# Performance work log

Measured on AMD Instinct MI355X. Metric: run time of the kernel, lower is better.

The kernel has to match this reference:

```python
import jax, jax.numpy as jnp
import numpy as np

ITERS = 8
LAMBDA0 = 0.01
PAD = 1.0
LR = 1.0
EPS = 1e-12


def _sobel_grads(fmap):
    # kornia spatial_gradient: normalized 3x3 sobel (/8), replicate padding. fmap: C,H,W
    kx = jnp.array([[-1., 0., 1.], [-2., 0., 2.], [-1., 0., 1.]], fmap.dtype) / 8.0
    k = jnp.stack([kx, kx.T])[:, None]                       # 2,1,3,3 (OIHW)
    f = jnp.pad(fmap, ((0, 0), (1, 1), (1, 1)), mode='edge')[:, None]  # C,1,H+2,W+2
    g = jax.lax.conv_general_dilated(f, k, (1, 1), 'VALID')  # C,2,H,W
    return g[:, 0], g[:, 1]


def _bilinear(tensor, pts):
    # grid_sample bilinear, align_corners=True, at pixel coords. tensor: C,H,W; pts: N,2 (x,y) -> N,C
    c, h, w = tensor.shape
    x, y = pts[:, 0], pts[:, 1]
    x0 = jnp.clip(jnp.floor(x), 0, w - 1)
    y0 = jnp.clip(jnp.floor(y), 0, h - 1)
    x1 = jnp.clip(x0 + 1, 0, w - 1)
    y1 = jnp.clip(y0 + 1, 0, h - 1)
    wx, wy = x - x0, y - y0
    x0i, x1i = x0.astype(jnp.int32), x1.astype(jnp.int32)
    y0i, y1i = y0.astype(jnp.int32), y1.astype(jnp.int32)
    v00 = tensor[:, y0i, x0i]
    v01 = tensor[:, y0i, x1i]
    v10 = tensor[:, y1i, x0i]
    v11 = tensor[:, y1i, x1i]
    out = (v00 * (1 - wx) * (1 - wy) + v01 * wx * (1 - wy)
           + v10 * (1 - wx) * wy + v11 * wx * wy)
    return out.T


def _skew(v):
    x, y, z = v[..., 0], v[..., 1], v[..., 2]
    o = jnp.zeros_like(x)
    return jnp.stack([o, -z, y, z, o, -x, -y, x, o], -1).reshape(v.shape[:-1] + (3, 3))


def _so3exp(w):
    theta = jnp.linalg.norm(w)
    small = theta < 1e-7
    th = jnp.where(small, 1.0, theta)
    A = jnp.where(small, 1.0, jnp.sin(th) / th)
    B = jnp.where(small, 0.5, (1.0 - jnp.cos(th)) / th ** 2)
    W = _skew(w)
    return jnp.eye(3, dtype=w.dtype) + A * W + B * (W @ W)


def _normalize(x):
    return x / jnp.maximum(jnp.linalg.norm(x, axis=-1, keepdims=True), EPS)


def _pnp(p3D, feature_ref, feature_query, K, R_init, t_init):
    C, H, W = feature_query.shape
    gx, gy = _sobel_grads(feature_query)
    fref = _normalize(feature_ref)
    fx, fy, cx, cy = K[0, 0], K[1, 1], K[0, 2], K[1, 2]
    f_scale = jnp.stack([fx, fy])
    c_off = jnp.stack([cx, cy])

    def project(R, t):
        p3q = p3D @ R.T + t
        pn = p3q[:, :2] / p3q[:, 2:3]
        return p3q, pn, pn * f_scale + c_off

    def in_image(p2):
        return ((p2[:, 0] >= PAD) & (p2[:, 0] < W - PAD)
                & (p2[:, 1] >= PAD) & (p2[:, 1] < H - PAD))

    def masked_cost(p2, vf):
        f = _normalize(_bilinear(feature_query, p2))
        cost = ((f - fref) ** 2).sum(-1)
        return (cost * vf).sum() / vf.sum()

    R, t = R_init, t_init
    lam = jnp.asarray(LAMBDA0, p3D.dtype)
    jacobi = None
    cost_best = None
    p2D_init = None

    for i in range(ITERS):
        p3q, pn, p2 = project(R, t)
        if i == 0:
            p2D_init = jax.lax.stop_gradient(p2)
        vf = in_image(p2).astype(p3D.dtype)  # mask-weight == gather of valid pts

        f_raw = _bilinear(feature_query, p2)  # N,C
        norm = jnp.maximum(jnp.linalg.norm(f_raw, axis=-1, keepdims=True), EPS)
        f = f_raw / norm
        error = f - fref
        if i == 0:
            cost_best = (((error ** 2).sum(-1)) * vf).sum() / vf.sum()

        # Jacobian chain: J = J_f_p2 @ J_p2_pn @ J_pn_p3 @ J_p3_T   -> N,C,6
        x_, y_, d = p3q[:, 0], p3q[:, 1], p3q[:, 2]
        z = jnp.zeros_like(d)
        Jpn = jnp.stack([1 / d, z, -x_ / d ** 2,
                         z, 1 / d, -y_ / d ** 2], -1).reshape(-1, 2, 3)
        Jpn = Jpn * f_scale[None, :, None]  # fold in J_p2_pn = diag(fx,fy)
        Jp3T = jnp.concatenate(
            [jnp.broadcast_to(jnp.eye(3, dtype=p3D.dtype), p3q.shape[:-1] + (3, 3)),
             -_skew(p3q)], -1)  # N,3,6
        J26 = Jpn @ Jp3T       # N,2,6

        Jf = jnp.stack([_bilinear(gx, p2), _bilinear(gy, p2)], -1)  # N,C,2
        # normalize-feat Jacobian (I - f f^T)/||f_raw||, fused (no NxCxC)
        proj = jnp.einsum('nc,nck->nk', f, Jf)
        Jf = (Jf - f[:, :, None] * proj[:, None, :]) / norm[:, :, None]

        J = Jf @ J26  # N,C,6
        if i == 0:
            jacobi = 1.0 / (1.0 + jnp.linalg.norm(J * vf[:, None, None], axis=(0, 1)))
        J = J * jacobi

        Grad = jnp.einsum('ncj,nc,n->j', J, error, vf)
        Hess = jnp.einsum('nci,ncj,n->ij', J, J, vf)

        damp = jnp.diag(jnp.diagonal(Hess) + 1e-9) * lam  # LM damping
        delta = -LR * jnp.linalg.solve(Hess + damp, Grad)
        delta = delta * jacobi
        dt, dw = delta[:3], delta[3:6]
        dr = _so3exp(dw)
        R_new, t_new = dr @ R, dr @ t + dt

        _, _, p2_new = project(R_new, t_new)
        vf_new = in_image(p2_new).astype(p3D.dtype)
        cost_new = masked_cost(p2_new, vf_new)

        accept = cost_new <= cost_best
        lam = jnp.clip(lam * jnp.where(accept, 0.1, 10.0), 1e-8, 1e4)
        R = jnp.where(accept, R_new, R)
        t = jnp.where(accept, t_new, t)
        cost_best = jnp.where(accept, cost_new, cost_best)

    p3D_sg = jax.lax.stop_gradient(p3D)
    pf = p3D_sg @ R.T + t
    p2f = (pf[:, :2] / pf[:, 2:3]) * f_scale + c_off
    f_i = _normalize(_bilinear(feature_query, p2D_init))
    f_f = _normalize(_bilinear(feature_query, p2f))
    cost_init = ((fref - f_i) ** 2).sum(-1)
    cost_final = ((fref - f_f) ** 2).sum(-1)
    nan = jnp.asarray(jnp.nan, cost_init.dtype)
    cost_init = jnp.where(in_image(p2D_init), cost_init, nan)
    cost_final = jnp.where(in_image(p2f), cost_final, nan)
    return R, t, cost_init, cost_final


def setup_inputs() -> dict:
    N, C, H, W = 10000, 128, 512, 512
    key = jax.random.key(0)
    ks = jax.random.split(key, 4)
    xy = jax.random.uniform(ks[0], (N, 2), jnp.float32, -2.0, 2.0)
    z = jax.random.uniform(ks[1], (N, 1), jnp.float32, 4.0, 10.0)
    p3D = jnp.concatenate([xy, z], -1)
    feature_query = jax.random.normal(ks[2], (C, H, W), jnp.float32) * 0.5
    feature_ref = jax.random.normal(ks[3], (N, C), jnp.float32)
    K = jnp.array([[500., 0., 256.], [0., 500., 256.], [0., 0., 1.]], jnp.float32)
    R_init = _so3exp(jnp.array([0.01, -0.02, 0.015], jnp.float32))
    t_init = jnp.array([0.05, -0.03, 0.10], jnp.float32)
    return {"p3D": p3D, "feature_ref": feature_ref, "feature_query": feature_query,
            "K": K, "R_init": R_init, "t_init": t_init}


def reference(p3D, feature_ref, feature_query, K, R_init, t_init):
    return _pnp(p3D, feature_ref, feature_query, K, R_init, t_init)
```

## Files before the change

### kernel.cpp

```cpp
#include <hip/hip_runtime.h>
#include <hip/hip_fp16.h>
#include <math.h>

#define HW_ (512*512)

typedef float vf4 __attribute__((ext_vector_type(4)));

__device__ __forceinline__ float wred(float v){
#pragma unroll
  for (int o = 32; o > 0; o >>= 1) v += __shfl_xor(v, o, 64);
  return v;
}

template<bool TR>
__device__ __forceinline__ float2 tap(const void* __restrict__ f, int y, int x, int c0){
  if (TR){
    const __half2* p = (const __half2*)f + (((size_t)((y << 9) + x)) << 6) + (c0 >> 1);
    return __half22float2(*p);
  } else {
    const float* ff = (const float*)f;
    int base = (y << 9) + x;
    float2 r;
    r.x = ff[(size_t)c0 * HW_ + base];
    r.y = ff[(size_t)(c0 + 1) * HW_ + base];
    return r;
  }
}

__device__ __forceinline__ void fgrad(const float P[16], float w00, float w01, float w10, float w11,
                                      float& f, float& gx, float& gy){
  f = w00*P[5] + w01*P[6] + w10*P[9] + w11*P[10];
  float gx11 = (P[2]  + 2.f*P[6]  + P[10] - P[0] - 2.f*P[4]  - P[8] ) * 0.125f;
  float gx12 = (P[3]  + 2.f*P[7]  + P[11] - P[1] - 2.f*P[5]  - P[9] ) * 0.125f;
  float gx21 = (P[6]  + 2.f*P[10] + P[14] - P[4] - 2.f*P[8]  - P[12]) * 0.125f;
  float gx22 = (P[7]  + 2.f*P[11] + P[15] - P[5] - 2.f*P[9]  - P[13]) * 0.125f;
  gx = w00*gx11 + w01*gx12 + w10*gx21 + w11*gx22;
  float gy11 = (P[8]  + 2.f*P[9]  + P[10] - P[0] - 2.f*P[1]  - P[2] ) * 0.125f;
  float gy12 = (P[9]  + 2.f*P[10] + P[11] - P[1] - 2.f*P[2]  - P[3] ) * 0.125f;
  float gy21 = (P[12] + 2.f*P[13] + P[14] - P[4] - 2.f*P[5]  - P[6] ) * 0.125f;
  float gy22 = (P[13] + 2.f*P[14] + P[15] - P[5] - 2.f*P[6]  - P[7] ) * 0.125f;
  gy = w00*gy11 + w01*gy12 + w10*gy21 + w11*gy22;
}

template<bool TR>
__device__ __forceinline__ float cost_point(const void* __restrict__ fmap,
                                            const float* __restrict__ frn,
                                            int n, float px, float py, int lane){
  int c0 = 2 * lane;
  float x0f = fminf(fmaxf(floorf(px), 0.f), 511.f);
  float y0f = fminf(fmaxf(floorf(py), 0.f), 511.f);
  int x0 = (int)x0f, y0 = (int)y0f;
  int x1 = min(x0 + 1, 511), y1 = min(y0 + 1, 511);
  float wx = px - x0f, wy = py - y0f;
  float w00 = (1.f-wx)*(1.f-wy), w01 = wx*(1.f-wy), w10 = (1.f-wx)*wy, w11 = wx*wy;
  float2 a = tap<TR>(fmap, y0, x0, c0), b = tap<TR>(fmap, y0, x1, c0);
  float2 c = tap<TR>(fmap, y1, x0, c0), d = tap<TR>(fmap, y1, x1, c0);
  float f0 = w00*a.x + w01*b.x + w10*c.x + w11*d.x;
  float f1 = w00*a.y + w01*b.y + w10*c.y + w11*d.y;
  float nrm = fmaxf(sqrtf(wred(f0*f0 + f1*f1)), 1e-12f);
  const float2 fr = *(const float2*)(frn + (size_t)n*128 + c0);
  float e0 = f0/nrm - fr.x;
  float e1 = f1/nrm - fr.y;
  return wred(e0*e0 + e1*e1);
}

__global__ __launch_bounds__(256) void transpose_kernel(const float* __restrict__ fq,
                                                        __half* __restrict__ ftr){
  __shared__ float tf[256 * 32];
  int g  = blockIdx.x & 3;
  int sb = (blockIdx.x >> 2) << 8;
  int t = threadIdx.x;
  int l = t & 63, w = t >> 6;
  int s = l >> 4;
  int ipg = (l & 15) + (w << 4);
  int px0 = ipg << 2;
#pragma unroll
  for (int p = 0; p < 8; p++){
    int ch = s * 8 + p;
    const vf4* src = (const vf4*)(fq + (size_t)(g*32 + ch) * HW_ + sb + px0);
    vf4 v = __builtin_nontemporal_load(src);
#pragma unroll
    for (int j = 0; j < 4; j++){
      int px = px0 + j;
      int fz = ((3 * (px >> 2)) + ((px & 3) << 3)) & 31;
      tf[px * 32 + (ch ^ fz)] = v[j];
    }
  }
  __syncthreads();
#pragma unroll
  for (int q = 0; q < 4; q++){
    int px = (q << 6) + (t >> 2);
    int c8 = (t & 3) << 3;
    int fz = ((3 * (px >> 2)) + ((px & 3) << 3)) & 31;
    float v[8];
#pragma unroll
    for (int j = 0; j < 8; j++) v[j] = tf[px * 32 + ((c8 + j) ^ fz)];
    __half2 hh[4];
    hh[0] = __floats2half2_rn(v[0], v[1]);
    hh[1] = __floats2half2_rn(v[2], v[3]);
    hh[2] = __floats2half2_rn(v[4], v[5]);
    hh[3] = __floats2half2_rn(v[6], v[7]);
    *(uint4*)(ftr + ((size_t)(sb + px)) * 128 + g * 32 + c8) = *(uint4*)hh;
  }
}

__global__ __launch_bounds__(256) void prep_kernel(const float* __restrict__ fref,
                                                   float* __restrict__ frn,
                                                   const float* __restrict__ Rin,
                                                   const float* __restrict__ tin,
                                                   float* __restrict__ state, int N){
  if (blockIdx.x == 0){
    int t = threadIdx.x;
    if (t < 9) state[t] = Rin[t];
    if (t < 3) state[9 + t] = tin[t];
    if (t == 0) state[30] = 0.01f;
  }
  int lane = threadIdx.x & 63;
  int n = blockIdx.x * 4 + (threadIdx.x >> 6);
  if (n >= N) return;
  int c0 = 2 * lane;
  float2 fr = *(const float2*)(fref + (size_t)n*128 + c0);
  float rn = fmaxf(sqrtf(wred(fr.x*fr.x + fr.y*fr.y)), 1e-12f);
  float2 o; o.x = fr.x / rn; o.y = fr.y / rn;
  *(float2*)(frn + (size_t)n*128 + c0) = o;
}

template<bool TR>
__global__ __launch_bounds__(512) void eval_kernel(
    const float* __restrict__ p3D, const float* __restrict__ frn,
    const void* __restrict__ fmap, const float* __restrict__ Km,
    const float* __restrict__ state, int po, double* __restrict__ part, int N)
{
  int t = threadIdx.x;
  int lane = t & 63;
  int wv = t >> 6;
  int n = blockIdx.x * 8 + wv;
  double acc = 0.0;
  if (n < N){
    float fx = Km[0], fy = Km[4], cx = Km[2], cy = Km[5];
    float R0=state[po+0],R1=state[po+1],R2=state[po+2],R3=state[po+3],R4=state[po+4];
    float R5=state[po+5],R6=state[po+6],R7=state[po+7],R8=state[po+8];
    float t0=state[po+9], t1=state[po+10], t2=state[po+11];
    float PX = p3D[3*n], PY = p3D[3*n+1], PZ = p3D[3*n+2];
    float X = R0*PX + R1*PY + R2*PZ + t0;
    float Y = R3*PX + R4*PY + R5*PZ + t1;
    float D = R6*PX + R7*PY + R8*PZ + t2;
    float px = X / D * fx + cx;
    float py = Y / D * fy + cy;
    if (px >= 1.f && px < 511.f && py >= 1.f && py < 511.f){
      int c0 = 2 * lane;
      float x0f = fminf(fmaxf(floorf(px), 0.f), 511.f);
      float y0f = fminf(fmaxf(floorf(py), 0.f), 511.f);
      int x0 = (int)x0f, y0 = (int)y0f;
      int x1 = min(x0 + 1, 511), y1 = min(y0 + 1, 511);
      float wx = px - x0f, wy = py - y0f;
      int xs[4] = {max(x0-1,0), x0, x1, min(x1+1,511)};
      int ys[4] = {max(y0-1,0), y0, y1, min(y1+1,511)};
      float Pa[16], Pb[16];
#pragma unroll
      for (int r = 0; r < 4; r++)
#pragma unroll
        for (int scol = 0; scol < 4; scol++){
          float2 v = tap<TR>(fmap, ys[r], xs[scol], c0);
          Pa[r*4+scol] = v.x; Pb[r*4+scol] = v.y;
        }
      float w00 = (1.f-wx)*(1.f-wy), w01 = wx*(1.f-wy), w10 = (1.f-wx)*wy, w11 = wx*wy;
      float f0, gx0, gy0, f1, gx1, gy1;
      fgrad(Pa, w00, w01, w10, w11, f0, gx0, gy0);
      fgrad(Pb, w00, w01, w10, w11, f1, gx1, gy1);
      float nrm = fmaxf(sqrtf(wred(f0*f0 + f1*f1)), 1e-12f);
      float fc0 = f0 / nrm, fc1 = f1 / nrm;
      float projx = wred(fc0*gx0 + fc1*gx1);
      float projy = wred(fc0*gy0 + fc1*gy1);
      float jx0 = (gx0 - fc0*projx) / nrm, jx1 = (gx1 - fc1*projx) / nrm;
      float jy0 = (gy0 - fc0*projy) / nrm, jy1 = (gy1 - fc1*projy) / nrm;
      const float2 fr2 = *(const float2*)(frn + (size_t)n*128 + c0);
      float e0 = fc0 - fr2.x, e1 = fc1 - fr2.y;
      float se2 = wred(e0*e0 + e1*e1);
      float gex = wred(jx0*e0 + jx1*e1);
      float gey = wred(jy0*e0 + jy1*e1);
      float sxx = wred(jx0*jx0 + jx1*jx1);
      float sxy = wred(jx0*jy0 + jx1*jy1);
      float syy = wred(jy0*jy0 + jy1*jy1);
      float invD = 1.f / D;
      float rx = X * invD, ry = Y * invD;
      float A[6] = {fx*invD, 0.f, -fx*rx*invD, -fx*rx*ry, fx*(1.f+rx*rx), -fx*ry};
      float B[6] = {0.f, fy*invD, -fy*ry*invD, -fy*(1.f+ry*ry), fy*rx*ry, fy*rx};
      int li = 0, lj = 0;
      {
        const int pi_[21] = {0,0,0,0,0,0,1,1,1,1,1,2,2,2,2,3,3,3,4,4,5};
        const int pj_[21] = {0,1,2,3,4,5,1,2,3,4,5,2,3,4,5,3,4,5,4,5,5};
        if (lane >= 6 && lane < 27){ li = pi_[lane-6]; lj = pj_[lane-6]; }
      }
      float val = 0.f;
      if (lane < 6)        val = A[lane]*gex + B[lane]*gey;
      else if (lane < 27)  val = A[li]*A[lj]*sxx + (A[li]*B[lj] + A[lj]*B[li])*sxy + B[li]*B[lj]*syy;
      else if (lane == 27) val = se2;
      else if (lane == 28) val = 1.f;
      acc = (double)val;
    }
  }
  __shared__ double red[8][32];
  if (lane < 32) red[wv][lane] = acc;
  __syncthreads();
  if (t < 32){
    double s = 0.0;
#pragma unroll
    for (int i = 0; i < 8; i++) s += red[i][t];
    part[(size_t)blockIdx.x * 32 + t] = s;
  }
}

__device__ void solve_step(const double* __restrict__ cur, float* __restrict__ state){
  const int pi_[21] = {0,0,0,0,0,0,1,1,1,1,1,2,2,2,2,3,3,3,4,4,5};
  const int pj_[21] = {0,1,2,3,4,5,1,2,3,4,5,2,3,4,5,3,4,5,4,5,5};
  double rg[6]; for (int i = 0; i < 6; i++) rg[i] = cur[i];
  double rh[6][6];
  for (int k = 0; k < 21; k++){ rh[pi_[k]][pj_[k]] = cur[6+k]; rh[pj_[k]][pi_[k]] = cur[6+k]; }
  float jac[6];
  for (int j = 0; j < 6; j++) jac[j] = state[24+j];
  double lam = (double)state[30];
  double H[6][7];
  for (int i = 0; i < 6; i++)
    for (int j = 0; j < 6; j++) H[i][j] = (double)jac[i] * (double)jac[j] * rh[i][j];
  for (int i = 0; i < 6; i++) H[i][i] += (H[i][i] + 1e-9) * lam;
  for (int i = 0; i < 6; i++) H[i][6] = -((double)jac[i] * rg[i]);
  for (int k = 0; k < 6; k++){
    int p = k; double mx = fabs(H[k][k]);
    for (int r = k+1; r < 6; r++) if (fabs(H[r][k]) > mx){ mx = fabs(H[r][k]); p = r; }
    if (p != k) for (int c = k; c < 7; c++){ double tmp = H[k][c]; H[k][c] = H[p][c]; H[p][c] = tmp; }
    double inv = 1.0 / H[k][k];
    for (int r = k+1; r < 6; r++){
      double m = H[r][k] * inv;
      for (int c = k; c < 7; c++) H[r][c] -= m * H[k][c];
    }
  }
  double d[6];
  for (int i = 5; i >= 0; i--){
    double sx = H[i][6];
    for (int c = i+1; c < 6; c++) sx -= H[i][c] * d[c];
    d[i] = sx / H[i][i];
  }
  for (int j = 0; j < 6; j++) d[j] *= (double)jac[j];
  double wx = d[3], wy = d[4], wz = d[5];
  double th2 = wx*wx + wy*wy + wz*wz, th = sqrt(th2);
  double Aa, Bb;
  if (th < 1e-7){ Aa = 1.0; Bb = 0.5; } else { Aa = sin(th)/th; Bb = (1.0 - cos(th))/th2; }
  double W[3][3] = {{0,-wz,wy},{wz,0,-wx},{-wy,wx,0}};
  double W2[3][3];
  for (int i = 0; i < 3; i++) for (int j = 0; j < 3; j++){
    double q = 0; for (int k = 0; k < 3; k++) q += W[i][k]*W[k][j]; W2[i][j] = q;
  }
  double dr[3][3];
  for (int i = 0; i < 3; i++) for (int j = 0; j < 3; j++)
    dr[i][j] = (i == j ? 1.0 : 0.0) + Aa*W[i][j] + Bb*W2[i][j];
  double Rc[3][3], tc[3];
  for (int i = 0; i < 3; i++){ tc[i] = state[9+i]; for (int j = 0; j < 3; j++) Rc[i][j] = state[i*3+j]; }
  for (int i = 0; i < 3; i++){
    for (int j = 0; j < 3; j++){
      double q = 0; for (int k = 0; k < 3; k++) q += dr[i][k]*Rc[k][j];
      state[12 + i*3 + j] = (float)q;
    }
    double q = 0; for (int k = 0; k < 3; k++) q += dr[i][k]*tc[k];
    state[21 + i] = (float)(q + d[i]);
  }
}

__global__ __launch_bounds__(1024) void update_kernel(
    const double* __restrict__ part, int rows, float* __restrict__ state,
    double* __restrict__ cur, int iter)
{
  __shared__ double sm[32*32];
  __shared__ double tot[32];
  int t = threadIdx.x;
  int l = t & 31, ch = t >> 5;
  double s = 0.0;
  for (int r = ch; r < rows; r += 32) s += part[(size_t)r*32 + l];
  sm[ch*32 + l] = s;
  __syncthreads();
  if (t < 32){
    double x = 0.0;
    for (int c = 0; c < 32; c++) x += sm[c*32 + t];
    tot[t] = x;
  }
  __syncthreads();
  if (t != 0) return;

  if (iter < 0){
    const int diag_k[6] = {0, 6, 11, 15, 18, 20};
    for (int j = 0; j < 6; j++)
      state[24+j] = 1.0f / (1.0f + (float)sqrt(tot[6 + diag_k[j]]));
    state[31] = (float)(tot[27] / tot[28]);
    for (int k = 0; k < 32; k++) cur[k] = tot[k];
    solve_step(cur, state);
  } else {
    float cn = (float)(tot[27] / tot[28]);
    bool acpt = (cn <= state[31]);
    float lam = state[30] * (acpt ? 0.1f : 10.f);
    state[30] = fminf(fmaxf(lam, 1e-8f), 1e4f);
    if (acpt){
      for (int i = 0; i < 12; i++) state[i] = state[12+i];
      state[31] = cn;
      for (int k = 0; k < 32; k++) cur[k] = tot[k];
    }
    if (iter < 7) solve_step(cur, state);
  }
}

template<bool TR>
__global__ __launch_bounds__(256) void final_kernel(
    const float* __restrict__ p3D, const float* __restrict__ frn,
    const void* __restrict__ fmap, const float* __restrict__ Km,
    const float* __restrict__ Rin, const float* __restrict__ tin,
    const float* __restrict__ state, float* __restrict__ out, int N)
{
  if (blockIdx.x == 0 && threadIdx.x < 12) out[threadIdx.x] = state[threadIdx.x];
  int lane = threadIdx.x & 63;
  int n = blockIdx.x * 4 + (threadIdx.x >> 6);
  if (n >= N) return;
  float fx = Km[0], fy = Km[4], cx = Km[2], cy = Km[5];
  float PX = p3D[3*n], PY = p3D[3*n+1], PZ = p3D[3*n+2];
  const float nanv = __int_as_float(0x7fc00000);
  {
    float X = Rin[0]*PX + Rin[1]*PY + Rin[2]*PZ + tin[0];
    float Y = Rin[3]*PX + Rin[4]*PY + Rin[5]*PZ + tin[1];
    float D = Rin[6]*PX + Rin[7]*PY + Rin[8]*PZ + tin[2];
    float px = X / D * fx + cx, py = Y / D * fy + cy;
    bool vf = (px >= 1.f && px < 511.f && py >= 1.f && py < 511.f);
    float ci = nanv;
    if (vf) ci = cost_point<TR>(fmap, frn, n, px, py, lane);
    if (lane == 0) out[12 + n] = ci;
  }
  {
    float X = state[0]*PX + state[1]*PY + state[2]*PZ + state[9];
    float Y = state[3]*PX + state[4]*PY + state[5]*PZ + state[10];
    float D = state[6]*PX + state[7]*PY + state[8]*PZ + state[11];
    float px = X / D * fx + cx, py = Y / D * fy + cy;
    bool vf = (px >= 1.f && px < 511.f && py >= 1.f && py < 511.f);
    float cf = nanv;
    if (vf) cf = cost_point<TR>(fmap, frn, n, px, py, lane);
    if (lane == 0) out[12 + N + n] = cf;
  }
}

extern "C" void kernel_launch(void* const* d_in, const int* in_sizes, int n_in,
                              void* d_out, int out_size, void* d_ws, size_t ws_size,
                              hipStream_t stream)
{
  const float* p3D  = (const float*)d_in[0];
  const float* fref = (const float*)d_in[1];
  const float* fq   = (const float*)d_in[2];
  const float* Km   = (const float*)d_in[3];
  const float* Rin  = (const float*)d_in[4];
  const float* tin  = (const float*)d_in[5];
  float* out = (float*)d_out;
  int N = in_sizes[0] / 3;
  int NBLK  = (N + 7) / 8;
  int NBLK4 = (N + 3) / 4;

  char* w = (char*)d_ws;
  float*  state = (float*)w;
  double* cur   = (double*)(w + 256);
  size_t part_bytes = (size_t)NBLK * 32 * 8;
  double* part = (double*)(w + 512);
  float* frn = (float*)(w + 512 + part_bytes);
  size_t frn_bytes = (size_t)N * 128 * 4;
  size_t ftr_off = (512 + part_bytes + frn_bytes + 255) & ~(size_t)255;
  __half* ftr = (__half*)(w + ftr_off);
  size_t need = ftr_off + (size_t)HW_ * 128 * 2;
  bool tr = (ws_size >= need);

  if (tr) transpose_kernel<<<(HW_/256)*4, 256, 0, stream>>>(fq, ftr);
  const void* fmap = tr ? (const void*)ftr : (const void*)fq;
  prep_kernel<<<NBLK4, 256, 0, stream>>>(fref, frn, Rin, tin, state, N);

  if (tr) eval_kernel<true ><<<NBLK, 512, 0, stream>>>(p3D, frn, fmap, Km, state, 0, part, N);
  else    eval_kernel<false><<<NBLK, 512, 0, stream>>>(p3D, frn, fmap, Km, state, 0, part, N);
  update_kernel<<<1, 1024, 0, stream>>>(part, NBLK, state, cur, -1);

  for (int it = 0; it < 8; it++){
    if (tr) eval_kernel<true ><<<NBLK, 512, 0, stream>>>(p3D, frn, fmap, Km, state, 12, part, N);
    else    eval_kernel<false><<<NBLK, 512, 0, stream>>>(p3D, frn, fmap, Km, state, 12, part, N);
    update_kernel<<<1, 1024, 0, stream>>>(part, NBLK, state, cur, it);
  }
  if (tr) final_kernel<true ><<<NBLK4, 256, 0, stream>>>(p3D, frn, fmap, Km, Rin, tin, state, out, N);
  else    final_kernel<false><<<NBLK4, 256, 0, stream>>>(p3D, frn, fmap, Km, Rin, tin, state, out, N);
}
```

Measured before the change: 480.6 us.

## Fuse the per-iteration update into eval kernel via last-block atomic reduction

Removes the separate single-block update_kernel launch after each eval pass. Each eval block instead bumps an atomic counter, and the last block to finish reduces the partials and runs the LM solve step in place. This saves 9 kernel launches and the idle gaps between them. The cost is a threadfence and an atomic per block, plus a tail in which one 512-thread block does the reduction.

```diff
diff --git a/kernel.cpp b/kernel.cpp
--- a/kernel.cpp
+++ b/kernel.cpp
@@ -108,12 +108,14 @@
                                                    float* __restrict__ frn,
                                                    const float* __restrict__ Rin,
                                                    const float* __restrict__ tin,
-                                                   float* __restrict__ state, int N){
+                                                   float* __restrict__ state,
+                                                   unsigned int* __restrict__ ctr, int N){
   if (blockIdx.x == 0){
     int t = threadIdx.x;
     if (t < 9) state[t] = Rin[t];
     if (t < 3) state[9 + t] = tin[t];
     if (t == 0) state[30] = 0.01f;
+    if (t < 16) ctr[t] = 0u;
   }
   int lane = threadIdx.x & 63;
   int n = blockIdx.x * 4 + (threadIdx.x >> 6);
@@ -125,11 +127,67 @@
   *(float2*)(frn + (size_t)n*128 + c0) = o;
 }
 
+__device__ void solve_step(const double* __restrict__ cur, float* __restrict__ state){
+  const int pi_[21] = {0,0,0,0,0,0,1,1,1,1,1,2,2,2,2,3,3,3,4,4,5};
+  const int pj_[21] = {0,1,2,3,4,5,1,2,3,4,5,2,3,4,5,3,4,5,4,5,5};
+  double rg[6]; for (int i = 0; i < 6; i++) rg[i] = cur[i];
+  double rh[6][6];
+  for (int k = 0; k < 21; k++){ rh[pi_[k]][pj_[k]] = cur[6+k]; rh[pj_[k]][pi_[k]] = cur[6+k]; }
+  float jac[6];
+  for (int j = 0; j < 6; j++) jac[j] = state[24+j];
+  double lam = (double)state[30];
+  double H[6][7];
+  for (int i = 0; i < 6; i++)
+    for (int j = 0; j < 6; j++) H[i][j] = (double)jac[i] * (double)jac[j] * rh[i][j];
+  for (int i = 0; i < 6; i++) H[i][i] += (H[i][i] + 1e-9) * lam;
+  for (int i = 0; i < 6; i++) H[i][6] = -((double)jac[i] * rg[i]);
+  for (int k = 0; k < 6; k++){
+    int p = k; double mx = fabs(H[k][k]);
+    for (int r = k+1; r < 6; r++) if (fabs(H[r][k]) > mx){ mx = fabs(H[r][k]); p = r; }
+    if (p != k) for (int c = k; c < 7; c++){ double tmp = H[k][c]; H[k][c] = H[p][c]; H[p][c] = tmp; }
+    double inv = 1.0 / H[k][k];
+    for (int r = k+1; r < 6; r++){
+      double m = H[r][k] * inv;
+      for (int c = k; c < 7; c++) H[r][c] -= m * H[k][c];
+    }
+  }
+  double d[6];
+  for (int i = 5; i >= 0; i--){
+    double sx = H[i][6];
+    for (int c = i+1; c < 6; c++) sx -= H[i][c] * d[c];
+    d[i] = sx / H[i][i];
+  }
+  for (int j = 0; j < 6; j++) d[j] *= (double)jac[j];
+  double wx = d[3], wy = d[4], wz = d[5];
+  double th2 = wx*wx + wy*wy + wz*wz, th = sqrt(th2);
+  double Aa, Bb;
+  if (th < 1e-7){ Aa = 1.0; Bb = 0.5; } else { Aa = sin(th)/th; Bb = (1.0 - cos(th))/th2; }
+  double W[3][3] = {{0,-wz,wy},{wz,0,-wx},{-wy,wx,0}};
+  double W2[3][3];
+  for (int i = 0; i < 3; i++) for (int j = 0; j < 3; j++){
+    double q = 0; for (int k = 0; k < 3; k++) q += W[i][k]*W[k][j]; W2[i][j] = q;
+  }
+  double dr[3][3];
+  for (int i = 0; i < 3; i++) for (int j = 0; j < 3; j++)
+    dr[i][j] = (i == j ? 1.0 : 0.0) + Aa*W[i][j] + Bb*W2[i][j];
+  double Rc[3][3], tc[3];
+  for (int i = 0; i < 3; i++){ tc[i] = state[9+i]; for (int j = 0; j < 3; j++) Rc[i][j] = state[i*3+j]; }
+  for (int i = 0; i < 3; i++){
+    for (int j = 0; j < 3; j++){
+      double q = 0; for (int k = 0; k < 3; k++) q += dr[i][k]*Rc[k][j];
+      state[12 + i*3 + j] = (float)q;
+    }
+    double q = 0; for (int k = 0; k < 3; k++) q += dr[i][k]*tc[k];
+    state[21 + i] = (float)(q + d[i]);
+  }
+}
+
 template<bool TR>
 __global__ __launch_bounds__(512) void eval_kernel(
     const float* __restrict__ p3D, const float* __restrict__ frn,
     const void* __restrict__ fmap, const float* __restrict__ Km,
-    const float* __restrict__ state, int po, double* __restrict__ part, int N)
+    float* __restrict__ state, int po, double* __restrict__ part,
+    double* __restrict__ cur, unsigned int* __restrict__ ctr, int iter, int N)
 {
   int t = threadIdx.x;
   int lane = t & 63;
@@ -209,78 +267,29 @@
     for (int i = 0; i < 8; i++) s += red[i][t];
     part[(size_t)blockIdx.x * 32 + t] = s;
   }
-}
-
-__device__ void solve_step(const double* __restrict__ cur, float* __restrict__ state){
-  const int pi_[21] = {0,0,0,0,0,0,1,1,1,1,1,2,2,2,2,3,3,3,4,4,5};
-  const int pj_[21] = {0,1,2,3,4,5,1,2,3,4,5,2,3,4,5,3,4,5,4,5,5};
-  double rg[6]; for (int i = 0; i < 6; i++) rg[i] = cur[i];
-  double rh[6][6];
-  for (int k = 0; k < 21; k++){ rh[pi_[k]][pj_[k]] = cur[6+k]; rh[pj_[k]][pi_[k]] = cur[6+k]; }
-  float jac[6];
-  for (int j = 0; j < 6; j++) jac[j] = state[24+j];
-  double lam = (double)state[30];
-  double H[6][7];
-  for (int i = 0; i < 6; i++)
-    for (int j = 0; j < 6; j++) H[i][j] = (double)jac[i] * (double)jac[j] * rh[i][j];
-  for (int i = 0; i < 6; i++) H[i][i] += (H[i][i] + 1e-9) * lam;
-  for (int i = 0; i < 6; i++) H[i][6] = -((double)jac[i] * rg[i]);
-  for (int k = 0; k < 6; k++){
-    int p = k; double mx = fabs(H[k][k]);
-    for (int r = k+1; r < 6; r++) if (fabs(H[r][k]) > mx){ mx = fabs(H[r][k]); p = r; }
-    if (p != k) for (int c = k; c < 7; c++){ double tmp = H[k][c]; H[k][c] = H[p][c]; H[p][c] = tmp; }
-    double inv = 1.0 / H[k][k];
-    for (int r = k+1; r < 6; r++){
-      double m = H[r][k] * inv;
-      for (int c = k; c < 7; c++) H[r][c] -= m * H[k][c];
-    }
-  }
-  double d[6];
-  for (int i = 5; i >= 0; i--){
-    double sx = H[i][6];
-    for (int c = i+1; c < 6; c++) sx -= H[i][c] * d[c];
-    d[i] = sx / H[i][i];
-  }
-  for (int j = 0; j < 6; j++) d[j] *= (double)jac[j];
-  double wx = d[3], wy = d[4], wz = d[5];
-  double th2 = wx*wx + wy*wy + wz*wz, th = sqrt(th2);
-  double Aa, Bb;
-  if (th < 1e-7){ Aa = 1.0; Bb = 0.5; } else { Aa = sin(th)/th; Bb = (1.0 - cos(th))/th2; }
-  double W[3][3] = {{0,-wz,wy},{wz,0,-wx},{-wy,wx,0}};
-  double W2[3][3];
-  for (int i = 0; i < 3; i++) for (int j = 0; j < 3; j++){
-    double q = 0; for (int k = 0; k < 3; k++) q += W[i][k]*W[k][j]; W2[i][j] = q;
-  }
-  double dr[3][3];
-  for (int i = 0; i < 3; i++) for (int j = 0; j < 3; j++)
-    dr[i][j] = (i == j ? 1.0 : 0.0) + Aa*W[i][j] + Bb*W2[i][j];
-  double Rc[3][3], tc[3];
-  for (int i = 0; i < 3; i++){ tc[i] = state[9+i]; for (int j = 0; j < 3; j++) Rc[i][j] = state[i*3+j]; }
-  for (int i = 0; i < 3; i++){
-    for (int j = 0; j < 3; j++){
-      double q = 0; for (int k = 0; k < 3; k++) q += dr[i][k]*Rc[k][j];
-      state[12 + i*3 + j] = (float)q;
-    }
-    double q = 0; for (int k = 0; k < 3; k++) q += dr[i][k]*tc[k];
-    state[21 + i] = (float)(q + d[i]);
-  }
-}
-
-__global__ __launch_bounds__(1024) void update_kernel(
-    const double* __restrict__ part, int rows, float* __restrict__ state,
-    double* __restrict__ cur, int iter)
-{
-  __shared__ double sm[32*32];
+
+  __shared__ int lastFlag;
+  if (t == 0){
+    __threadfence();
+    unsigned int done = atomicAdd(&ctr[iter + 1], 1u);
+    lastFlag = (done == gridDim.x - 1u) ? 1 : 0;
+  }
+  __syncthreads();
+  if (!lastFlag) return;
+  __threadfence();
+
+  __shared__ double sm[16*32];
   __shared__ double tot[32];
-  int t = threadIdx.x;
-  int l = t & 31, ch = t >> 5;
+  int l = t & 31, r0 = t >> 5;
+  int rows = gridDim.x;
   double s = 0.0;
-  for (int r = ch; r < rows; r += 32) s += part[(size_t)r*32 + l];
-  sm[ch*32 + l] = s;
+  for (int r = r0; r < rows; r += 16) s += part[(size_t)r*32 + l];
+  sm[r0*32 + l] = s;
   __syncthreads();
   if (t < 32){
     double x = 0.0;
-    for (int c = 0; c < 32; c++) x += sm[c*32 + t];
+#pragma unroll
+    for (int c = 0; c < 16; c++) x += sm[c*32 + t];
     tot[t] = x;
   }
   __syncthreads();
@@ -359,29 +368,28 @@
   int NBLK4 = (N + 3) / 4;
 
   char* w = (char*)d_ws;
-  float*  state = (float*)w;
-  double* cur   = (double*)(w + 256);
+  float*        state = (float*)w;
+  double*       cur   = (double*)(w + 256);
+  unsigned int* ctr   = (unsigned int*)(w + 512);
+  double* part = (double*)(w + 768);
   size_t part_bytes = (size_t)NBLK * 32 * 8;
-  double* part = (double*)(w + 512);
-  float* frn = (float*)(w + 512 + part_bytes);
+  float* frn = (float*)(w + 768 + part_bytes);
   size_t frn_bytes = (size_t)N * 128 * 4;
-  size_t ftr_off = (512 + part_bytes + frn_bytes + 255) & ~(size_t)255;
+  size_t ftr_off = (768 + part_bytes + frn_bytes + 255) & ~(size_t)255;
   __half* ftr = (__half*)(w + ftr_off);
   size_t need = ftr_off + (size_t)HW_ * 128 * 2;
   bool tr = (ws_size >= need);
 
   if (tr) transpose_kernel<<<(HW_/256)*4, 256, 0, stream>>>(fq, ftr);
   const void* fmap = tr ? (const void*)ftr : (const void*)fq;
-  prep_kernel<<<NBLK4, 256, 0, stream>>>(fref, frn, Rin, tin, state, N);
-
-  if (tr) eval_kernel<true ><<<NBLK, 512, 0, stream>>>(p3D, frn, fmap, Km, state, 0, part, N);
-  else    eval_kernel<false><<<NBLK, 512, 0, stream>>>(p3D, frn, fmap, Km, state, 0, part, N);
-  update_kernel<<<1, 1024, 0, stream>>>(part, NBLK, state, cur, -1);
+  prep_kernel<<<NBLK4, 256, 0, stream>>>(fref, frn, Rin, tin, state, ctr, N);
+
+  if (tr) eval_kernel<true ><<<NBLK, 512, 0, stream>>>(p3D, frn, fmap, Km, state, 0, part, cur, ctr, -1, N);
+  else    eval_kernel<false><<<NBLK, 512, 0, stream>>>(p3D, frn, fmap, Km, state, 0, part, cur, ctr, -1, N);
 
   for (int it = 0; it < 8; it++){
-    if (tr) eval_kernel<true ><<<NBLK, 512, 0, stream>>>(p3D, frn, fmap, Km, state, 12, part, N);
-    else    eval_kernel<false><<<NBLK, 512, 0, stream>>>(p3D, frn, fmap, Km, state, 12, part, N);
-    update_kernel<<<1, 1024, 0, stream>>>(part, NBLK, state, cur, it);
+    if (tr) eval_kernel<true ><<<NBLK, 512, 0, stream>>>(p3D, frn, fmap, Km, state, 12, part, cur, ctr, it, N);
+    else    eval_kernel<false><<<NBLK, 512, 0, stream>>>(p3D, frn, fmap, Km, state, 12, part, cur, ctr, it, N);
   }
   if (tr) final_kernel<true ><<<NBLK4, 256, 0, stream>>>(p3D, frn, fmap, Km, Rin, tin, state, out, N);
   else    final_kernel<false><<<NBLK4, 256, 0, stream>>>(p3D, frn, fmap, Km, Rin, tin, state, out, N);
```

New measurement: 805.3 us. 1.68x slower.

## Batch wave reductions algebraically and reuse initial eval for initial cost

Applied to the files above, without the earlier changes.

Rewrites the normalized residual, gradient and Hessian terms as functions of independent raw dot products (f·f, f·fr, f·g, g·g, etc.). All ten wave reductions can then run without the serial dependency on the norm. The first eval pass also writes per-point initial cost directly, so final_kernel no longer resamples at the initial pose. This costs a few more reductions per point, and the expanded algebra may round slightly differently from the direct normalized form.

```diff
diff --git a/kernel.cpp b/kernel.cpp
--- a/kernel.cpp
+++ b/kernel.cpp
@@ -57,11 +57,13 @@
   float2 c = tap<TR>(fmap, y1, x0, c0), d = tap<TR>(fmap, y1, x1, c0);
   float f0 = w00*a.x + w01*b.x + w10*c.x + w11*d.x;
   float f1 = w00*a.y + w01*b.y + w10*c.y + w11*d.y;
-  float nrm = fmaxf(sqrtf(wred(f0*f0 + f1*f1)), 1e-12f);
   const float2 fr = *(const float2*)(frn + (size_t)n*128 + c0);
-  float e0 = f0/nrm - fr.x;
-  float e1 = f1/nrm - fr.y;
-  return wred(e0*e0 + e1*e1);
+  float Sff  = wred(f0*f0 + f1*f1);
+  float Sffr = wred(f0*fr.x + f1*fr.y);
+  float Sfr  = wred(fr.x*fr.x + fr.y*fr.y);
+  float nrm = fmaxf(sqrtf(Sff), 1e-12f);
+  float inv = 1.f / nrm;
+  return Sff*inv*inv - 2.f*Sffr*inv + Sfr;
 }
 
 __global__ __launch_bounds__(256) void transpose_kernel(const float* __restrict__ fq,
@@ -129,7 +131,8 @@
 __global__ __launch_bounds__(512) void eval_kernel(
     const float* __restrict__ p3D, const float* __restrict__ frn,
     const void* __restrict__ fmap, const float* __restrict__ Km,
-    const float* __restrict__ state, int po, double* __restrict__ part, int N)
+    const float* __restrict__ state, int po, double* __restrict__ part,
+    float* __restrict__ cost_out, int N)
 {
   int t = threadIdx.x;
   int lane = t & 63;
@@ -147,7 +150,8 @@
     float D = R6*PX + R7*PY + R8*PZ + t2;
     float px = X / D * fx + cx;
     float py = Y / D * fy + cy;
-    if (px >= 1.f && px < 511.f && py >= 1.f && py < 511.f){
+    bool valid = (px >= 1.f && px < 511.f && py >= 1.f && py < 511.f);
+    if (valid){
       int c0 = 2 * lane;
       float x0f = fminf(fmaxf(floorf(px), 0.f), 511.f);
       float y0f = fminf(fmaxf(floorf(py), 0.f), 511.f);
@@ -168,20 +172,25 @@
       float f0, gx0, gy0, f1, gx1, gy1;
       fgrad(Pa, w00, w01, w10, w11, f0, gx0, gy0);
       fgrad(Pb, w00, w01, w10, w11, f1, gx1, gy1);
-      float nrm = fmaxf(sqrtf(wred(f0*f0 + f1*f1)), 1e-12f);
-      float fc0 = f0 / nrm, fc1 = f1 / nrm;
-      float projx = wred(fc0*gx0 + fc1*gx1);
-      float projy = wred(fc0*gy0 + fc1*gy1);
-      float jx0 = (gx0 - fc0*projx) / nrm, jx1 = (gx1 - fc1*projx) / nrm;
-      float jy0 = (gy0 - fc0*projy) / nrm, jy1 = (gy1 - fc1*projy) / nrm;
       const float2 fr2 = *(const float2*)(frn + (size_t)n*128 + c0);
-      float e0 = fc0 - fr2.x, e1 = fc1 - fr2.y;
-      float se2 = wred(e0*e0 + e1*e1);
-      float gex = wred(jx0*e0 + jx1*e1);
-      float gey = wred(jy0*e0 + jy1*e1);
-      float sxx = wred(jx0*jx0 + jx1*jx1);
-      float sxy = wred(jx0*jy0 + jx1*jy1);
-      float syy = wred(jy0*jy0 + jy1*jy1);
+      float Sff   = wred(f0*f0   + f1*f1);
+      float Sffr  = wred(f0*fr2.x + f1*fr2.y);
+      float Sfr   = wred(fr2.x*fr2.x + fr2.y*fr2.y);
+      float Sfgx  = wred(f0*gx0  + f1*gx1);
+      float Sfgy  = wred(f0*gy0  + f1*gy1);
+      float Sgxfr = wred(gx0*fr2.x + gx1*fr2.y);
+      float Sgyfr = wred(gy0*fr2.x + gy1*fr2.y);
+      float Sgxgx = wred(gx0*gx0 + gx1*gx1);
+      float Sgxgy = wred(gx0*gy0 + gx1*gy1);
+      float Sgygy = wred(gy0*gy0 + gy1*gy1);
+      float nrm = fmaxf(sqrtf(Sff), 1e-12f);
+      float inv = 1.f/nrm, inv2 = inv*inv, inv3 = inv2*inv, inv4 = inv2*inv2;
+      float se2 = Sff*inv2 - 2.f*Sffr*inv + Sfr;
+      float gex = Sfgx*inv2 - Sgxfr*inv - Sfgx*Sff*inv4 + Sfgx*Sffr*inv3;
+      float gey = Sfgy*inv2 - Sgyfr*inv - Sfgy*Sff*inv4 + Sfgy*Sffr*inv3;
+      float sxx = Sgxgx*inv2 - Sfgx*Sfgx*inv4;
+      float sxy = Sgxgy*inv2 - Sfgx*Sfgy*inv4;
+      float syy = Sgygy*inv2 - Sfgy*Sfgy*inv4;
       float invD = 1.f / D;
       float rx = X * invD, ry = Y * invD;
       float A[6] = {fx*invD, 0.f, -fx*rx*invD, -fx*rx*ry, fx*(1.f+rx*rx), -fx*ry};
@@ -198,6 +207,9 @@
       else if (lane == 27) val = se2;
       else if (lane == 28) val = 1.f;
       acc = (double)val;
+      if (cost_out && lane == 0) cost_out[n] = se2;
+    } else if (cost_out && lane == 0){
+      cost_out[n] = __int_as_float(0x7fc00000);
     }
   }
   __shared__ double red[8][32];
@@ -311,7 +323,6 @@
 __global__ __launch_bounds__(256) void final_kernel(
     const float* __restrict__ p3D, const float* __restrict__ frn,
     const void* __restrict__ fmap, const float* __restrict__ Km,
-    const float* __restrict__ Rin, const float* __restrict__ tin,
     const float* __restrict__ state, float* __restrict__ out, int N)
 {
   if (blockIdx.x == 0 && threadIdx.x < 12) out[threadIdx.x] = state[threadIdx.x];
@@ -320,27 +331,14 @@
   if (n >= N) return;
   float fx = Km[0], fy = Km[4], cx = Km[2], cy = Km[5];
   float PX = p3D[3*n], PY = p3D[3*n+1], PZ = p3D[3*n+2];
-  const float nanv = __int_as_float(0x7fc00000);
-  {
-    float X = Rin[0]*PX + Rin[1]*PY + Rin[2]*PZ + tin[0];
-    float Y = Rin[3]*PX + Rin[4]*PY + Rin[5]*PZ + tin[1];
-    float D = Rin[6]*PX + Rin[7]*PY + Rin[8]*PZ + tin[2];
-    float px = X / D * fx + cx, py = Y / D * fy + cy;
-    bool vf = (px >= 1.f && px < 511.f && py >= 1.f && py < 511.f);
-    float ci = nanv;
-    if (vf) ci = cost_point<TR>(fmap, frn, n, px, py, lane);
-    if (lane == 0) out[12 + n] = ci;
-  }
-  {
-    float X = state[0]*PX + state[1]*PY + state[2]*PZ + state[9];
-    float Y = state[3]*PX + state[4]*PY + state[5]*PZ + state[10];
-    float D = state[6]*PX + state[7]*PY + state[8]*PZ + state[11];
-    float px = X / D * fx + cx, py = Y / D * fy + cy;
-    bool vf = (px >= 1.f && px < 511.f && py >= 1.f && py < 511.f);
-    float cf = nanv;
-    if (vf) cf = cost_point<TR>(fmap, frn, n, px, py, lane);
-    if (lane == 0) out[12 + N + n] = cf;
-  }
+  float X = state[0]*PX + state[1]*PY + state[2]*PZ + state[9];
+  float Y = state[3]*PX + state[4]*PY + state[5]*PZ + state[10];
+  float D = state[6]*PX + state[7]*PY + state[8]*PZ + state[11];
+  float px = X / D * fx + cx, py = Y / D * fy + cy;
+  bool vf = (px >= 1.f && px < 511.f && py >= 1.f && py < 511.f);
+  float cf = __int_as_float(0x7fc00000);
+  if (vf) cf = cost_point<TR>(fmap, frn, n, px, py, lane);
+  if (lane == 0) out[12 + N + n] = cf;
 }
 
 extern "C" void kernel_launch(void* const* d_in, const int* in_sizes, int n_in,
@@ -361,8 +359,8 @@
   char* w = (char*)d_ws;
   float*  state = (float*)w;
   double* cur   = (double*)(w + 256);
+  double* part  = (double*)(w + 512);
   size_t part_bytes = (size_t)NBLK * 32 * 8;
-  double* part = (double*)(w + 512);
   float* frn = (float*)(w + 512 + part_bytes);
   size_t frn_bytes = (size_t)N * 128 * 4;
   size_t ftr_off = (512 + part_bytes + frn_bytes + 255) & ~(size_t)255;
@@ -374,15 +372,15 @@
   const void* fmap = tr ? (const void*)ftr : (const void*)fq;
   prep_kernel<<<NBLK4, 256, 0, stream>>>(fref, frn, Rin, tin, state, N);
 
-  if (tr) eval_kernel<true ><<<NBLK, 512, 0, stream>>>(p3D, frn, fmap, Km, state, 0, part, N);
-  else    eval_kernel<false><<<NBLK, 512, 0, stream>>>(p3D, frn, fmap, Km, state, 0, part, N);
+  if (tr) eval_kernel<true ><<<NBLK, 512, 0, stream>>>(p3D, frn, fmap, Km, state, 0, part, out + 12, N);
+  else    eval_kernel<false><<<NBLK, 512, 0, stream>>>(p3D, frn, fmap, Km, state, 0, part, out + 12, N);
   update_kernel<<<1, 1024, 0, stream>>>(part, NBLK, state, cur, -1);
 
   for (int it = 0; it < 8; it++){
-    if (tr) eval_kernel<true ><<<NBLK, 512, 0, stream>>>(p3D, frn, fmap, Km, state, 12, part, N);
-    else    eval_kernel<false><<<NBLK, 512, 0, stream>>>(p3D, frn, fmap, Km, state, 12, part, N);
+    if (tr) eval_kernel<true ><<<NBLK, 512, 0, stream>>>(p3D, frn, fmap, Km, state, 12, part, nullptr, N);
+    else    eval_kernel<false><<<NBLK, 512, 0, stream>>>(p3D, frn, fmap, Km, state, 12, part, nullptr, N);
     update_kernel<<<1, 1024, 0, stream>>>(part, NBLK, state, cur, it);
   }
-  if (tr) final_kernel<true ><<<NBLK4, 256, 0, stream>>>(p3D, frn, fmap, Km, Rin, tin, state, out, N);
-  else    final_kernel<false><<<NBLK4, 256, 0, stream>>>(p3D, frn, fmap, Km, Rin, tin, state, out, N);
-}
+  if (tr) final_kernel<true ><<<NBLK4, 256, 0, stream>>>(p3D, frn, fmap, Km, state, out, N);
+  else    final_kernel<false><<<NBLK4, 256, 0, stream>>>(p3D, frn, fmap, Km, state, out, N);
+}
```

New measurement: 476.4 us. No clear change (-0.9%).
